# Kernel tuning notes

Measured on AMD Instinct MI355X. Metric: run time of the kernel, lower is better.

Reference implementation:

```python
import jax, jax.numpy as jnp
import numpy as np

B, T, D, M = 4, 4096, 2048, 512


def setup_inputs() -> dict:
    key = jax.random.key(0)
    ks = jax.random.split(key, 6)
    x = jax.random.normal(ks[0], (B, T, D), dtype=jnp.float32)
    memory_state = jnp.zeros((B, M), dtype=jnp.float32)
    # xavier_normal-style init for the linear layers, zero biases
    Wv = jax.random.normal(ks[1], (M, D), dtype=jnp.float32) * np.float32(np.sqrt(2.0 / (D + M)))
    bv = jnp.zeros((M,), dtype=jnp.float32)
    Wg = jax.random.normal(ks[2], (D, D + M), dtype=jnp.float32) * np.float32(np.sqrt(2.0 / (2 * D + M)))
    bg = jnp.zeros((D,), dtype=jnp.float32)
    time_decay = jax.random.normal(ks[3], (M,), dtype=jnp.float32) * 0.01
    time_first = jax.random.normal(ks[4], (M,), dtype=jnp.float32) * 0.01
    return dict(x=x, memory_state=memory_state, Wv=Wv, bv=bv, Wg=Wg, bg=bg,
                time_decay=time_decay, time_first=time_first)


def reference(x, memory_state, Wv, bv, Wg, bg, time_decay, time_first):
    # v = value_proj(x): [B, T, M]
    v = jnp.einsum('btd,md->btm', x, Wv) + bv
    decay = jax.nn.sigmoid(time_decay) * 0.9 + 0.1   # [M]
    first = jax.nn.sigmoid(time_first)               # [M]

    # Recurrence: s_0 = memory_state; wv_t = v_t + s_t*first; s_{t+1} = s_t*decay + v_t
    def step(s, v_t):
        wv_t = v_t + s * first
        return s * decay + v_t, wv_t

    v_tb = jnp.swapaxes(v, 0, 1)                     # [T, B, M] for scan over time
    next_memory, wv_tb = jax.lax.scan(step, memory_state, v_tb)
    weighted_values = jnp.swapaxes(wv_tb, 0, 1)      # [B, T, M]

    # output = x + output_gate(concat[x, weighted_values])
    combined = jnp.concatenate([x, weighted_values], axis=-1)  # [B, T, D+M]
    output = x + jnp.einsum('btk,dk->btd', combined, Wg) + bg
    return output, next_memory
```

## Files before the change

### kernel.cpp

```cpp
#include <hip/hip_runtime.h>
#include <hip/hip_bf16.h>
#include <cstdint>
#include <cstddef>

#define B_DIM 4
#define T_DIM 4096
#define D_DIM 2048
#define M_DIM 512
#define NTOK  (B_DIM * T_DIM)
#define KCOMB (D_DIM + M_DIM)
#define NCHUNK 64
#define CLEN   64

typedef __attribute__((ext_vector_type(8)))  __bf16 bf16x8;
typedef __attribute__((ext_vector_type(16))) float  f32x16;

__device__ __forceinline__ unsigned short f2bf(float f) {
  union { float f; unsigned u; } v; v.f = f;
  unsigned r = v.u + 0x7fffu + ((v.u >> 16) & 1u);
  return (unsigned short)(r >> 16);
}

__device__ __forceinline__ float sigmoidf(float x) { return 1.0f / (1.0f + expf(-x)); }

#define XBLK  ((NTOK * D_DIM / 4) / 256)
#define WVBLK ((M_DIM * D_DIM / 4) / 256)
#define WGBLK ((D_DIM * KCOMB / 4) / 256)
__global__ void cast_all_kernel(const float* __restrict__ x, const float* __restrict__ Wv,
                                const float* __restrict__ Wg,
                                unsigned short* __restrict__ comb,
                                unsigned short* __restrict__ WvB,
                                unsigned short* __restrict__ WgB) {
  int bid = blockIdx.x;
  const float* src; unsigned short* dst; size_t soff, doff;
  if (bid < XBLK) {
    int idx = bid * 256 + threadIdx.x;
    int n = idx >> 9;
    int c = (idx & 511) << 2;
    src = x;   soff = (size_t)n * D_DIM + c;
    dst = comb; doff = (size_t)n * KCOMB + c;
  } else if (bid < XBLK + WVBLK) {
    int idx = (bid - XBLK) * 256 + threadIdx.x;
    src = Wv;  soff = (size_t)idx * 4;
    dst = WvB; doff = (size_t)idx * 4;
  } else {
    int idx = (bid - XBLK - WVBLK) * 256 + threadIdx.x;
    src = Wg;  soff = (size_t)idx * 4;
    dst = WgB; doff = (size_t)idx * 4;
  }
  float4 v = *(const float4*)(src + soff);
  ushort4 o;
  o.x = f2bf(v.x); o.y = f2bf(v.y); o.z = f2bf(v.z); o.w = f2bf(v.w);
  *(ushort4*)(dst + doff) = o;
}

__global__ __launch_bounds__(M_DIM) void recur_partial(
    const float* __restrict__ v, const float* __restrict__ td, float* __restrict__ P) {
  int m = threadIdx.x;
  int b = blockIdx.x >> 6;
  int c = blockIdx.x & (NCHUNK - 1);
  float decay = sigmoidf(td[m]) * 0.9f + 0.1f;
  const float* vp = v + ((size_t)(b * T_DIM + c * CLEN)) * M_DIM + m;
  float p = 0.0f;
  for (int t0 = 0; t0 < CLEN; t0 += 8) {
    float vt[8];
#pragma unroll
    for (int u = 0; u < 8; ++u) vt[u] = vp[(size_t)(t0 + u) * M_DIM];
#pragma unroll
    for (int u = 0; u < 8; ++u) p = p * decay + vt[u];
  }
  P[(size_t)blockIdx.x * M_DIM + m] = p;
}

__global__ __launch_bounds__(M_DIM) void recur_apply(
    const float* __restrict__ v, const float* __restrict__ mem0,
    const float* __restrict__ td, const float* __restrict__ tf,
    const float* __restrict__ P,
    unsigned short* __restrict__ comb, float* __restrict__ nmem) {
  int m = threadIdx.x;
  int b = blockIdx.x >> 6;
  int c = blockIdx.x & (NCHUNK - 1);
  float decay = sigmoidf(td[m]) * 0.9f + 0.1f;
  float first = sigmoidf(tf[m]);
  float dL = decay;
  dL = dL * dL; dL = dL * dL; dL = dL * dL; dL = dL * dL; dL = dL * dL; dL = dL * dL;

  float s = mem0[b * M_DIM + m];
  const float* Pp = P + (size_t)(b * NCHUNK) * M_DIM + m;
  for (int ci = 0; ci < c; ++ci)
    s = s * dL + Pp[(size_t)ci * M_DIM];

  const float* vp = v + ((size_t)(b * T_DIM + c * CLEN)) * M_DIM + m;
  unsigned short* wp = comb + ((size_t)(b * T_DIM + c * CLEN)) * KCOMB + D_DIM + m;
  for (int t0 = 0; t0 < CLEN; t0 += 8) {
    float vt[8];
#pragma unroll
    for (int u = 0; u < 8; ++u) vt[u] = vp[(size_t)(t0 + u) * M_DIM];
#pragma unroll
    for (int u = 0; u < 8; ++u) {
      wp[(size_t)(t0 + u) * KCOMB] = f2bf(vt[u] + s * first);
      s = s * decay + vt[u];
    }
  }
  if (c == NCHUNK - 1) nmem[b * M_DIM + m] = s;
}

#define BM 128
#define BN 128
#define BK 64

template <bool ADD_X, int MODE>
__global__ __launch_bounds__(256) void gemm_bt(
    const unsigned short* __restrict__ A, int lda,
    const unsigned short* __restrict__ B, int ldb,
    const float* __restrict__ bias, const float* __restrict__ xadd,
    float* __restrict__ C, int N, int K) {
  const int tid = threadIdx.x;
  const int lane = tid & 63;
  const int wave = tid >> 6;
  const int wm = (wave >> 1) * 64;
  const int wn = (wave & 1) * 64;
  const int l31 = lane & 31;
  const int half = lane >> 5;

  int tileM, tileN;
  {
    int idx = blockIdx.x;
    int xcd = idx & 7, local = idx >> 3;
    if (MODE == 1) {
      tileN = (xcd * 2 + (local & 1)) * BN;
      tileM = (local >> 1) * BM;
    } else {
      tileM = (xcd * 16 + (local >> 2)) * BM;
      tileN = (local & 3) * BN;
    }
  }

  __shared__ unsigned short As[BM * BK];
  __shared__ unsigned short Bs[BN * BK];

  f32x16 acc[2][2] = {};

  for (int k0 = 0; k0 < K; k0 += BK) {
#pragma unroll
    for (int j = 0; j < 4; ++j) {
      int c = j * 256 + tid;
      int row = c >> 3;
      int kc = c & 7;
      int gkc = kc ^ (row & 7);
      const unsigned short* gA = A + (size_t)(tileM + row) * lda + k0 + gkc * 8;
      const unsigned short* gB = B + (size_t)(tileN + row) * ldb + k0 + gkc * 8;
      __builtin_amdgcn_global_load_lds((const __attribute__((address_space(1))) void*)gA,
                                       (__attribute__((address_space(3))) void*)(As + c * 8),
                                       16, 0, 0);
      __builtin_amdgcn_global_load_lds((const __attribute__((address_space(1))) void*)gB,
                                       (__attribute__((address_space(3))) void*)(Bs + c * 8),
                                       16, 0, 0);
    }
    __syncthreads();

#pragma unroll
    for (int s = 0; s < 4; ++s) {
      const int g = s * 2 + half;
      bf16x8 af[2], bfr[2];
#pragma unroll
      for (int i = 0; i < 2; ++i) {
        int ra = wm + i * 32 + l31;
        int rb = wn + i * 32 + l31;
        af[i]  = *(const bf16x8*)(As + ra * BK + ((g ^ (ra & 7)) * 8));
        bfr[i] = *(const bf16x8*)(Bs + rb * BK + ((g ^ (rb & 7)) * 8));
      }
#pragma unroll
      for (int mi = 0; mi < 2; ++mi)
#pragma unroll
        for (int ni = 0; ni < 2; ++ni)
          acc[mi][ni] = __builtin_amdgcn_mfma_f32_32x32x16_bf16(af[mi], bfr[ni], acc[mi][ni], 0, 0, 0);
    }
    __syncthreads();
  }

#pragma unroll
  for (int mi = 0; mi < 2; ++mi) {
#pragma unroll
    for (int ni = 0; ni < 2; ++ni) {
      int col = tileN + wn + ni * 32 + l31;
      float bcol = bias[col];
#pragma unroll
      for (int r = 0; r < 16; ++r) {
        int row = tileM + wm + mi * 32 + 4 * half + (r & 3) + 8 * (r >> 2);
        float val = acc[mi][ni][r] + bcol;
        if (ADD_X) val += xadd[(size_t)row * N + col];
        C[(size_t)row * N + col] = val;
      }
    }
  }
}

#define BAR_FENCE() do { asm volatile("" ::: "memory"); \
  __builtin_amdgcn_s_barrier(); asm volatile("" ::: "memory"); } while (0)

template <bool ADD_X, int LDA, int LDB, int NOUT, int KTOT>
__global__ __launch_bounds__(512, 2) void gemm256_bt(
    const unsigned short* __restrict__ Amat,
    const unsigned short* __restrict__ Bmat,
    const float* __restrict__ bias,
    const float* __restrict__ xadd,
    float* __restrict__ C) {
  constexpr int NK  = KTOT / 64;
  constexpr int NI  = NK / 2;
  constexpr int NTN = NOUT / 256;
  constexpr int NWG = (NTOK / 256) * NTN;
  constexpr int PERX = NWG / 8;

  __shared__ unsigned short As[2][256 * 64];
  __shared__ unsigned short Bs[2][256 * 64];

  const int tid  = threadIdx.x;
  const int lane = tid & 63;
  const int half = lane >> 5;
  const int l31  = lane & 31;
  const int wave = tid >> 6;
  const int wrow = (wave >> 2) * 128;
  const int wcol = (wave & 3) * 64;

  const int bid   = blockIdx.x;
  const int wgid  = (bid & 7) * PERX + (bid >> 3);
  const int tileM = (wgid / NTN) * 256;
  const int tileN = (wgid % NTN) * 256;

  const int row_lo = tid >> 3;
  const int scol   = (((tid & 7) ^ (row_lo & 7)) << 3);
  const unsigned short* pA = Amat + (size_t)(tileM + row_lo) * LDA + scol;
  const unsigned short* pB = Bmat + (size_t)(tileN + row_lo) * LDB + scol;

#define STAGE_A(b, h, kt) do { \
  _Pragma("unroll") for (int j = 0; j < 2; ++j) { \
    const unsigned short* _s = pA + (size_t)((h) * 128 + j * 64) * LDA + (kt) * 64; \
    __builtin_amdgcn_global_load_lds((const __attribute__((address_space(1))) void*)_s, \
        (__attribute__((address_space(3))) void*)(&As[(b)][(h) * 8192 + (j * 512 + tid) * 8]), \
        16, 0, 0); \
  } \
} while (0)

#define STAGE_B(b, h, kt) do { \
  _Pragma("unroll") for (int j = 0; j < 2; ++j) { \
    const unsigned short* _s = pB + (size_t)((h) * 128 + j * 64) * LDB + (kt) * 64; \
    __builtin_amdgcn_global_load_lds((const __attribute__((address_space(1))) void*)_s, \
        (__attribute__((address_space(3))) void*)(&Bs[(b)][(h) * 8192 + (j * 512 + tid) * 8]), \
        16, 0, 0); \
  } \
} while (0)

  f32x16 acc[4][2] = {};
  bf16x8 af[2][4];
  bf16x8 bfr[2][2];

#define READ_A(b, mh) do { \
  _Pragma("unroll") for (int mi = 0; mi < 2; ++mi) { \
    const int _r = wrow + (mh) * 64 + mi * 32 + l31; \
    _Pragma("unroll") for (int s = 0; s < 4; ++s) \
      af[mi][s] = *(const bf16x8*)(&As[(b)][_r * 64 + (((s * 2 + half) ^ (_r & 7)) << 3)]); \
  } \
} while (0)

#define READ_BSP(b, sp) do { \
  _Pragma("unroll") for (int ni = 0; ni < 2; ++ni) { \
    const int _r = wcol + ni * 32 + l31; \
    _Pragma("unroll") for (int j = 0; j < 2; ++j) \
      bfr[ni][j] = *(const bf16x8*)(&Bs[(b)][_r * 64 + \
          (((((sp) * 2 + j) * 2 + half) ^ (_r & 7)) << 3)]); \
  } \
} while (0)

#define MFMA_Q(mh, sp) do { \
  _Pragma("unroll") for (int j = 0; j < 2; ++j) \
    _Pragma("unroll") for (int mi = 0; mi < 2; ++mi) \
      _Pragma("unroll") for (int ni = 0; ni < 2; ++ni) \
        acc[(mh) * 2 + mi][(ni)] = __builtin_amdgcn_mfma_f32_32x32x16_bf16( \
            af[mi][(sp) * 2 + j], bfr[ni][j], acc[(mh) * 2 + mi][(ni)], 0, 0, 0); \
} while (0)

#define PHASE_TAIL(mh, sp) do { \
  BAR_FENCE(); \
  asm volatile("s_waitcnt lgkmcnt(0)" ::: "memory"); \
  __builtin_amdgcn_sched_barrier(0); \
  __builtin_amdgcn_s_setprio(1); \
  MFMA_Q(mh, sp); \
  __builtin_amdgcn_s_setprio(0); \
  BAR_FENCE(); \
} while (0)

  STAGE_A(0, 0, 0); STAGE_A(0, 1, 0);
  STAGE_B(0, 0, 0); STAGE_B(0, 1, 0);
  STAGE_A(1, 0, 1); STAGE_A(1, 1, 1);
  asm volatile("s_waitcnt vmcnt(4)" ::: "memory");
  BAR_FENCE();

#define ITER(i2, FULL) do { \
   \
  READ_A(0, 0); READ_BSP(0, 0); \
  STAGE_B(1, 0, (i2) + 1); STAGE_B(1, 1, (i2) + 1); \
  PHASE_TAIL(0, 0); \
   \
  READ_BSP(0, 1); \
  PHASE_TAIL(0, 1); \
   \
  READ_A(0, 1); \
  PHASE_TAIL(1, 1); \
   \
  READ_BSP(0, 0); \
  if (FULL) { STAGE_A(0, 0, (i2) + 2); STAGE_A(0, 1, (i2) + 2); \
              asm volatile("s_waitcnt vmcnt(4)" ::: "memory"); } \
  else      { asm volatile("s_waitcnt vmcnt(0)" ::: "memory"); } \
  PHASE_TAIL(1, 0); \
   \
  READ_A(1, 0); READ_BSP(1, 0); \
  if (FULL) { STAGE_B(0, 0, (i2) + 2); STAGE_B(0, 1, (i2) + 2); } \
  PHASE_TAIL(0, 0); \
   \
  READ_BSP(1, 1); \
  PHASE_TAIL(0, 1); \
   \
  READ_A(1, 1); \
  PHASE_TAIL(1, 1); \
   \
  READ_BSP(1, 0); \
  if (FULL) { STAGE_A(1, 0, (i2) + 3); STAGE_A(1, 1, (i2) + 3); \
              asm volatile("s_waitcnt vmcnt(4)" ::: "memory"); } \
  PHASE_TAIL(1, 0); \
} while (0)

#pragma unroll 1
  for (int i = 0; i < NI - 1; ++i) ITER(2 * i, 1);
  ITER(2 * (NI - 1), 0);

#undef ITER
#undef PHASE_TAIL
#undef MFMA_Q
#undef READ_BSP
#undef READ_A
#undef STAGE_B
#undef STAGE_A

#pragma unroll
  for (int mq = 0; mq < 4; ++mq) {
#pragma unroll
    for (int ni = 0; ni < 2; ++ni) {
      const int col = tileN + wcol + ni * 32 + l31;
      const float bc = bias[col];
#pragma unroll
      for (int r = 0; r < 16; ++r) {
        const int row = tileM + wrow + mq * 32 + 4 * half + (r & 3) + 8 * (r >> 2);
        float val = acc[mq][ni][r] + bc;
        if (ADD_X) val += xadd[(size_t)row * NOUT + col];
        C[(size_t)row * NOUT + col] = val;
      }
    }
  }
}

extern "C" void kernel_launch(void* const* d_in, const int* in_sizes, int n_in,
                              void* d_out, int out_size, void* d_ws, size_t ws_size,
                              hipStream_t stream) {
  const float* x   = (const float*)d_in[0];
  const float* mem = (const float*)d_in[1];
  const float* Wv  = (const float*)d_in[2];
  const float* bv  = (const float*)d_in[3];
  const float* Wg  = (const float*)d_in[4];
  const float* bg  = (const float*)d_in[5];
  const float* td  = (const float*)d_in[6];
  const float* tf  = (const float*)d_in[7];
  float* out = (float*)d_out;

  char* ws = (char*)d_ws;
  unsigned short* comb = (unsigned short*)ws;
  float* v = (float*)(ws + (size_t)NTOK * KCOMB * 2);
  unsigned short* WvB = (unsigned short*)((char*)v + (size_t)NTOK * M_DIM * 4);
  unsigned short* WgB = (unsigned short*)((char*)WvB + (size_t)M_DIM * D_DIM * 2);
  float* P = (float*)WvB;

  cast_all_kernel<<<XBLK + WVBLK + WGBLK, 256, 0, stream>>>(x, Wv, Wg, comb, WvB, WgB);

  gemm_bt<false, 0><<<(NTOK / BM) * (M_DIM / BN), 256, 0, stream>>>(
      comb, KCOMB, WvB, D_DIM, bv, nullptr, v, M_DIM, D_DIM);

  recur_partial<<<B_DIM * NCHUNK, M_DIM, 0, stream>>>(v, td, P);
  recur_apply<<<B_DIM * NCHUNK, M_DIM, 0, stream>>>(
      v, mem, td, tf, P, comb, out + (size_t)NTOK * D_DIM);

  gemm256_bt<true, KCOMB, KCOMB, D_DIM, KCOMB>
      <<<(NTOK / 256) * (D_DIM / 256), 512, 0, stream>>>(comb, WgB, bg, x, out);
}
```

Baseline: 508.7 us.

## Switch GEMM inner loop from 32x32x16 to 16x16x32 MFMA with double-buffered B fragments

Rewrites the bf16 GEMM's register tiling to use 16x16x32 MFMA instructions, with 8x4 accumulator tiles per wave instead of 4x2. B fragments are split into two register sets (bf/bg), so some quadrants reuse already-loaded B and skip re-reading LDS. Partial lgkmcnt waits are added so MFMAs can start before all LDS reads land. Accumulator register count is unchanged, but the epilogue store pattern changes and the more numerous, smaller MFMAs may lower issue efficiency.

```diff
diff --git a/kernel.cpp b/kernel.cpp
--- a/kernel.cpp
+++ b/kernel.cpp
@@ -14,6 +14,7 @@
 
 typedef __attribute__((ext_vector_type(8)))  __bf16 bf16x8;
 typedef __attribute__((ext_vector_type(16))) float  f32x16;
+typedef __attribute__((ext_vector_type(4)))  float  f32x4;
 
 __device__ __forceinline__ unsigned short f2bf(float f) {
   union { float f; unsigned u; } v; v.f = f;
@@ -217,8 +218,8 @@
 
   const int tid  = threadIdx.x;
   const int lane = tid & 63;
-  const int half = lane >> 5;
-  const int l31  = lane & 31;
+  const int l15  = lane & 15;
+  const int g4   = lane >> 4;
   const int wave = tid >> 6;
   const int wrow = (wave >> 2) * 128;
   const int wcol = (wave & 3) * 64;
@@ -233,7 +234,7 @@
   const unsigned short* pA = Amat + (size_t)(tileM + row_lo) * LDA + scol;
   const unsigned short* pB = Bmat + (size_t)(tileN + row_lo) * LDB + scol;
 
-#define STAGE_A(b, h, kt) do { \
+#define GSTAGE_A(b, h, kt) do { \
   _Pragma("unroll") for (int j = 0; j < 2; ++j) { \
     const unsigned short* _s = pA + (size_t)((h) * 128 + j * 64) * LDA + (kt) * 64; \
     __builtin_amdgcn_global_load_lds((const __attribute__((address_space(1))) void*)_s, \
@@ -242,7 +243,7 @@
   } \
 } while (0)
 
-#define STAGE_B(b, h, kt) do { \
+#define GSTAGE_B(b, h, kt) do { \
   _Pragma("unroll") for (int j = 0; j < 2; ++j) { \
     const unsigned short* _s = pB + (size_t)((h) * 128 + j * 64) * LDB + (kt) * 64; \
     __builtin_amdgcn_global_load_lds((const __attribute__((address_space(1))) void*)_s, \
@@ -251,107 +252,107 @@
   } \
 } while (0)
 
-  f32x16 acc[4][2] = {};
-  bf16x8 af[2][4];
-  bf16x8 bfr[2][2];
-
-#define READ_A(b, mh) do { \
-  _Pragma("unroll") for (int mi = 0; mi < 2; ++mi) { \
-    const int _r = wrow + (mh) * 64 + mi * 32 + l31; \
-    _Pragma("unroll") for (int s = 0; s < 4; ++s) \
-      af[mi][s] = *(const bf16x8*)(&As[(b)][_r * 64 + (((s * 2 + half) ^ (_r & 7)) << 3)]); \
+  f32x4  acc[8][4] = {};
+  bf16x8 af[4][2];
+  bf16x8 bf[2][2];
+  bf16x8 bg[2][2];
+
+#define GREAD_A(b, mh) do { \
+  _Pragma("unroll") for (int mt = 0; mt < 4; ++mt) { \
+    const int _r = wrow + (mh) * 64 + mt * 16 + l15; \
+    _Pragma("unroll") for (int ks = 0; ks < 2; ++ks) \
+      af[mt][ks] = *(const bf16x8*)(&As[(b)][_r * 64 + (((ks * 4 + g4) ^ (_r & 7)) << 3)]); \
   } \
 } while (0)
 
-#define READ_BSP(b, sp) do { \
-  _Pragma("unroll") for (int ni = 0; ni < 2; ++ni) { \
-    const int _r = wcol + ni * 32 + l31; \
-    _Pragma("unroll") for (int j = 0; j < 2; ++j) \
-      bfr[ni][j] = *(const bf16x8*)(&Bs[(b)][_r * 64 + \
-          (((((sp) * 2 + j) * 2 + half) ^ (_r & 7)) << 3)]); \
+#define GREAD_B(b, nh, dst) do { \
+  _Pragma("unroll") for (int nt = 0; nt < 2; ++nt) { \
+    const int _r = wcol + (nh) * 32 + nt * 16 + l15; \
+    _Pragma("unroll") for (int ks = 0; ks < 2; ++ks) \
+      dst[nt][ks] = *(const bf16x8*)(&Bs[(b)][_r * 64 + (((ks * 4 + g4) ^ (_r & 7)) << 3)]); \
   } \
 } while (0)
 
-#define MFMA_Q(mh, sp) do { \
-  _Pragma("unroll") for (int j = 0; j < 2; ++j) \
-    _Pragma("unroll") for (int mi = 0; mi < 2; ++mi) \
-      _Pragma("unroll") for (int ni = 0; ni < 2; ++ni) \
-        acc[(mh) * 2 + mi][(ni)] = __builtin_amdgcn_mfma_f32_32x32x16_bf16( \
-            af[mi][(sp) * 2 + j], bfr[ni][j], acc[(mh) * 2 + mi][(ni)], 0, 0, 0); \
-} while (0)
-
-#define PHASE_TAIL(mh, sp) do { \
+#define GMFMA_Q(mh, nh, breg) do { \
+  _Pragma("unroll") for (int ks = 0; ks < 2; ++ks) \
+    _Pragma("unroll") for (int mt = 0; mt < 4; ++mt) \
+      _Pragma("unroll") for (int nt = 0; nt < 2; ++nt) \
+        acc[(mh) * 4 + mt][(nh) * 2 + nt] = __builtin_amdgcn_mfma_f32_16x16x32_bf16( \
+            af[mt][ks], breg[nt][ks], acc[(mh) * 4 + mt][(nh) * 2 + nt], 0, 0, 0); \
+} while (0)
+
+#define GTAIL(mh, nh, breg) do { \
   BAR_FENCE(); \
   asm volatile("s_waitcnt lgkmcnt(0)" ::: "memory"); \
   __builtin_amdgcn_sched_barrier(0); \
   __builtin_amdgcn_s_setprio(1); \
-  MFMA_Q(mh, sp); \
+  GMFMA_Q(mh, nh, breg); \
   __builtin_amdgcn_s_setprio(0); \
   BAR_FENCE(); \
 } while (0)
 
-  STAGE_A(0, 0, 0); STAGE_A(0, 1, 0);
-  STAGE_B(0, 0, 0); STAGE_B(0, 1, 0);
-  STAGE_A(1, 0, 1); STAGE_A(1, 1, 1);
+  GSTAGE_A(0, 0, 0); GSTAGE_A(0, 1, 0);
+  GSTAGE_B(0, 0, 0); GSTAGE_B(0, 1, 0);
+  GSTAGE_A(1, 0, 1); GSTAGE_A(1, 1, 1);
   asm volatile("s_waitcnt vmcnt(4)" ::: "memory");
   BAR_FENCE();
 
-#define ITER(i2, FULL) do { \
-   \
-  READ_A(0, 0); READ_BSP(0, 0); \
-  STAGE_B(1, 0, (i2) + 1); STAGE_B(1, 1, (i2) + 1); \
-  PHASE_TAIL(0, 0); \
-   \
-  READ_BSP(0, 1); \
-  PHASE_TAIL(0, 1); \
-   \
-  READ_A(0, 1); \
-  PHASE_TAIL(1, 1); \
-   \
-  READ_BSP(0, 0); \
-  if (FULL) { STAGE_A(0, 0, (i2) + 2); STAGE_A(0, 1, (i2) + 2); \
+#define GITER(i2, FULL) do { \
+   \
+  GREAD_A(0, 0); GREAD_B(0, 0, bf); \
+  GSTAGE_B(1, 0, (i2) + 1); GSTAGE_B(1, 1, (i2) + 1); \
+  asm volatile("s_waitcnt lgkmcnt(8)" ::: "memory"); \
+  GTAIL(0, 0, bf); \
+   \
+  GREAD_B(0, 1, bg); \
+  GTAIL(0, 1, bg); \
+   \
+  GREAD_A(0, 1); \
+  GTAIL(1, 1, bg); \
+   \
+  if (FULL) { GSTAGE_A(0, 0, (i2) + 2); GSTAGE_A(0, 1, (i2) + 2); \
               asm volatile("s_waitcnt vmcnt(4)" ::: "memory"); } \
   else      { asm volatile("s_waitcnt vmcnt(0)" ::: "memory"); } \
-  PHASE_TAIL(1, 0); \
-   \
-  READ_A(1, 0); READ_BSP(1, 0); \
-  if (FULL) { STAGE_B(0, 0, (i2) + 2); STAGE_B(0, 1, (i2) + 2); } \
-  PHASE_TAIL(0, 0); \
-   \
-  READ_BSP(1, 1); \
-  PHASE_TAIL(0, 1); \
-   \
-  READ_A(1, 1); \
-  PHASE_TAIL(1, 1); \
-   \
-  READ_BSP(1, 0); \
-  if (FULL) { STAGE_A(1, 0, (i2) + 3); STAGE_A(1, 1, (i2) + 3); \
+  GTAIL(1, 0, bf); \
+   \
+  GREAD_A(1, 0); GREAD_B(1, 0, bf); \
+  if (FULL) { GSTAGE_B(0, 0, (i2) + 2); GSTAGE_B(0, 1, (i2) + 2); } \
+  asm volatile("s_waitcnt lgkmcnt(8)" ::: "memory"); \
+  GTAIL(0, 0, bf); \
+   \
+  GREAD_B(1, 1, bg); \
+  GTAIL(0, 1, bg); \
+   \
+  GREAD_A(1, 1); \
+  GTAIL(1, 1, bg); \
+   \
+  if (FULL) { GSTAGE_A(1, 0, (i2) + 3); GSTAGE_A(1, 1, (i2) + 3); \
               asm volatile("s_waitcnt vmcnt(4)" ::: "memory"); } \
-  PHASE_TAIL(1, 0); \
+  GTAIL(1, 0, bf); \
 } while (0)
 
 #pragma unroll 1
-  for (int i = 0; i < NI - 1; ++i) ITER(2 * i, 1);
-  ITER(2 * (NI - 1), 0);
-
-#undef ITER
-#undef PHASE_TAIL
-#undef MFMA_Q
-#undef READ_BSP
-#undef READ_A
-#undef STAGE_B
-#undef STAGE_A
-
-#pragma unroll
-  for (int mq = 0; mq < 4; ++mq) {
-#pragma unroll
-    for (int ni = 0; ni < 2; ++ni) {
-      const int col = tileN + wcol + ni * 32 + l31;
+  for (int i = 0; i < NI - 1; ++i) GITER(2 * i, 1);
+  GITER(2 * (NI - 1), 0);
+
+#undef GITER
+#undef GTAIL
+#undef GMFMA_Q
+#undef GREAD_B
+#undef GREAD_A
+#undef GSTAGE_B
+#undef GSTAGE_A
+
+#pragma unroll
+  for (int mt = 0; mt < 8; ++mt) {
+#pragma unroll
+    for (int nt = 0; nt < 4; ++nt) {
+      const int col = tileN + wcol + nt * 16 + l15;
       const float bc = bias[col];
 #pragma unroll
-      for (int r = 0; r < 16; ++r) {
-        const int row = tileM + wrow + mq * 32 + 4 * half + (r & 3) + 8 * (r >> 2);
-        float val = acc[mq][ni][r] + bc;
+      for (int r = 0; r < 4; ++r) {
+        const int row = tileM + wrow + mt * 16 + g4 * 4 + r;
+        float val = acc[mt][nt][r] + bc;
         if (ADD_X) val += xadd[(size_t)row * NOUT + col];
         C[(size_t)row * NOUT + col] = val;
       }
```

New measurement: 508.1 us. No clear change (-0.1%).
